# Performance work log

Hardware: AMD Instinct MI355X
Metric: run time of the kernel (lower is better)

Reference implementation:

```python
import jax, jax.numpy as jnp
import numpy as np

EPS_LN = 1e-5
EPS_SM = 1e-16  # PyG softmax denominator epsilon


def setup_inputs() -> dict:
    key = jax.random.key(0)
    k1, k2, k3 = jax.random.split(key, 3)
    N = 100000          # total nodes
    Q, C = 4, 128       # num_querys, hidden_channels
    M = Q * C           # multi_hidden_channels = 512
    B = 512             # batch_size (num graphs)
    x = jax.random.normal(k1, (N, M), dtype=jnp.float32)
    W_nlin = jax.random.normal(k2, (M, M), dtype=jnp.float32) * 0.02
    b_nlin = jnp.zeros((M,), dtype=jnp.float32)
    querys = jnp.ones((Q, C), dtype=jnp.float32)  # q_scale = 1.0 fill
    graph_idx = jnp.sort(jax.random.randint(k3, (N,), 0, B, dtype=jnp.int32))
    return {"x": x, "W_nlin": W_nlin, "b_nlin": b_nlin, "querys": querys,
            "graph_idx": graph_idx, "batch_size": B}


def reference(x, W_nlin, b_nlin, querys, graph_idx, batch_size):
    Q, C = querys.shape
    # nlin: MLP(1 layer, multi_hidden_channels, act=True) -> Linear + ReLU
    h = jax.nn.relu(x @ W_nlin + b_nlin)          # [N, Q*C]
    h = h.reshape(-1, Q, C)                       # [N, Q, C]
    # LayerNorm over hidden_channels, no affine
    mu = jnp.mean(h, axis=-1, keepdims=True)
    var = jnp.mean(jnp.square(h - mu), axis=-1, keepdims=True)
    q = (h - mu) * jax.lax.rsqrt(var + EPS_LN) * querys[None]  # [N, Q, C]
    # segment softmax over nodes within each graph (elementwise in Q, C)
    seg_max = jax.ops.segment_max(q, graph_idx, num_segments=batch_size)  # [B, Q, C]
    e = jnp.exp(q - seg_max[graph_idx])
    seg_sum = jax.ops.segment_sum(e, graph_idx, num_segments=batch_size)
    a = e / (seg_sum[graph_idx] + EPS_SM)         # [N, Q, C]
    # weighted scatter-sum pooling per graph
    r = jax.ops.segment_sum(a * h, graph_idx, num_segments=batch_size)   # [B, Q, C]
    # out_method='lin' with n_agg_trans=0 -> agglin is identity
    return r.reshape(batch_size, -1)              # [B, Q*C]
```

## Files before the change

kernel.cpp:

```cpp
#include <hip/hip_runtime.h>
#include <hip/hip_bf16.h>
#include <stdint.h>

typedef __attribute__((ext_vector_type(8))) short bf16x8;
typedef __attribute__((ext_vector_type(4))) float f32x4;
typedef __attribute__((ext_vector_type(8))) unsigned short ushort8;

__device__ __forceinline__ unsigned short cvt1(float f) {
  union { __hip_bfloat16 b; unsigned short u; } v;
  v.b = __float2bfloat16(f);
  return v.u;
}

__device__ __forceinline__ void gld_lds16(const void* g, void* l) {
  __builtin_amdgcn_global_load_lds(
      (const __attribute__((address_space(1))) unsigned int*)g,
      (__attribute__((address_space(3))) unsigned int*)l,
      16, 0, 0);
}

#define SM_OFS 12.0f

__global__ void cast_wt_kernel(const float* __restrict__ W,
                               unsigned short* __restrict__ wt) {
  int t = blockIdx.x * blockDim.x + threadIdx.x;
  int n = t >> 9;
  int k = t & 511;
  wt[t] = cvt1(W[k * 512 + n]);
}

__global__ __launch_bounds__(256, 4) void gemm_fused_kernel(
    const float* __restrict__ x,
    const unsigned short* __restrict__ wt,
    const float* __restrict__ bias,
    const float* __restrict__ qs,
    const int* __restrict__ gidx,
    float* __restrict__ NU,
    float* __restrict__ SA,
    int N, int mtiles) {
  __shared__ __align__(16) char smem[8192 + 8192];
  char* AsB = smem;
  char* BsB = smem + 8192;

  const int nfull = (mtiles >> 3) << 3;
  const int full_bids = nfull * 4;
  int mtile, ntile;
  {
    const int bid = blockIdx.x;
    if (bid < full_bids) {
      const int chunk = bid >> 5, j = bid & 31;
      mtile = (chunk << 3) + (j & 7);
      ntile = j >> 3;
    } else {
      const int j = bid - full_bids;
      const int rem = mtiles - nfull;
      mtile = nfull + j % rem;
      ntile = j / rem;
    }
  }
  const int m0 = mtile << 6;
  const int n0 = ntile << 7;

  const int tid = threadIdx.x;
  const int lane = tid & 63;
  const int wid = tid >> 6;
  const int wr = wid >> 1;
  const int wc = wid & 1;

  f32x4 acc[2][4];
#pragma unroll
  for (int m = 0; m < 2; m++)
#pragma unroll
    for (int n = 0; n < 4; n++) acc[m][n] = (f32x4){0.f, 0.f, 0.f, 0.f};

  const float* aP[2];
  int aLds[2];
#pragma unroll
  for (int L = 0; L < 2; L++) {
    const int p = (L << 12) + tid * 16;
    const int row = p >> 7;
    const int slot = (p >> 4) & 7;
    const int k4 = slot ^ (row & 7);
    aP[L] = x + (long)min(m0 + row, N - 1) * 512 + k4 * 4;
    aLds[L] = (L << 12) + (wid << 10);
  }

  const unsigned short* bP[2];
  int bLds[2];
#pragma unroll
  for (int L = 0; L < 2; L++) {
    const int p = (L << 12) + tid * 16;
    const int row = p >> 6;
    const int slot = (p >> 4) & 3;
    const int k8 = slot ^ ((row >> 1) & 3);
    bP[L] = wt + (long)(n0 + row) * 512 + k8 * 8;
    bLds[L] = (L << 12) + (wid << 10);
  }

  const int rsel = lane & 15;
  const int k8l = lane >> 4;
  int offA[2], offB[4];
#pragma unroll
  for (int m = 0; m < 2; m++) {
    const int ra = wr * 32 + m * 16 + rsel;
    offA[m] = ra * 128 + (((k8l << 1) ^ (ra & 7)) << 4);
  }
#pragma unroll
  for (int n = 0; n < 4; n++) {
    const int rb = wc * 64 + n * 16 + rsel;
    offB[n] = rb * 64 + ((k8l ^ ((rb >> 1) & 3)) << 4);
  }

#pragma unroll
  for (int t = 0; t < 16; t++) {
#pragma unroll
    for (int L = 0; L < 2; L++) gld_lds16(aP[L] + (t << 5), AsB + aLds[L]);
#pragma unroll
    for (int L = 0; L < 2; L++) gld_lds16(bP[L] + (t << 5), BsB + bLds[L]);
    __syncthreads();

    bf16x8 af[2], bq[4];
#pragma unroll
    for (int m = 0; m < 2; m++) {
      const f32x4 r0 = *(const f32x4*)(AsB + offA[m]);
      const f32x4 r1 = *(const f32x4*)(AsB + (offA[m] ^ 16));
      ushort8 u;
      u[0] = cvt1(r0[0]); u[1] = cvt1(r0[1]);
      u[2] = cvt1(r0[2]); u[3] = cvt1(r0[3]);
      u[4] = cvt1(r1[0]); u[5] = cvt1(r1[1]);
      u[6] = cvt1(r1[2]); u[7] = cvt1(r1[3]);
      af[m] = (bf16x8)u;
    }
#pragma unroll
    for (int n = 0; n < 4; n++) bq[n] = *(const bf16x8*)(BsB + offB[n]);
#pragma unroll
    for (int m = 0; m < 2; m++)
#pragma unroll
      for (int n = 0; n < 4; n++)
        acc[m][n] = __builtin_amdgcn_mfma_f32_16x16x32_bf16(
            af[m], bq[n], acc[m][n], 0, 0, 0);
    __syncthreads();
  }

  int* sgidx = (int*)smem;
  float* sS = (float*)(smem + 256);
  float* sQ = (float*)(smem + 1024);

  if (tid < 64) {
    const long rg = (long)m0 + tid;
    sgidx[tid] = (rg < N) ? gidx[rg] : 0x7fffffff;
  }

  const int colb = n0 + wc * 64 + rsel;
  float bval[4], qsv[4];
#pragma unroll
  for (int n = 0; n < 4; n++) {
    bval[n] = bias[colb + n * 16];
    qsv[n] = qs[colb + n * 16];
  }

#pragma unroll
  for (int m = 0; m < 2; m++) {
#pragma unroll
    for (int i = 0; i < 4; i++) {
      const int row_l = wr * 32 + m * 16 + (k8l << 2) + i;
      float s = 0.f, q = 0.f;
#pragma unroll
      for (int n = 0; n < 4; n++) {
        float v = fmaxf(acc[m][n][i] + bval[n], 0.f);
        s += v;
        q += v * v;
      }
#pragma unroll
      for (int d = 1; d < 16; d <<= 1) {
        s += __shfl_xor(s, d, 64);
        q += __shfl_xor(q, d, 64);
      }
      if (rsel == 0) {
        sS[row_l * 2 + wc] = s;
        sQ[row_l * 2 + wc] = q;
      }
    }
  }
  __syncthreads();

  const int lastv = min(63, (int)((long)N - 1 - (long)m0));
  if (wr * 32 <= lastv) {
    const int gmin = sgidx[wr * 32];
    const int gmax = sgidx[min(wr * 32 + 31, lastv)];
    for (int g = gmin; g <= gmax; ++g) {
      float num[4] = {0.f, 0.f, 0.f, 0.f};
      float den[4] = {0.f, 0.f, 0.f, 0.f};
#pragma unroll
      for (int m = 0; m < 2; m++) {
#pragma unroll
        for (int i = 0; i < 4; i++) {
          const int row_l = wr * 32 + m * 16 + (k8l << 2) + i;
          if (sgidx[row_l] == g) {
            const float s = sS[row_l * 2] + sS[row_l * 2 + 1];
            const float qq = sQ[row_l * 2] + sQ[row_l * 2 + 1];
            const float mean = s * (1.f / 128.f);
            const float var = qq * (1.f / 128.f) - mean * mean;
            const float rstd = rsqrtf(var + 1e-5f);
#pragma unroll
            for (int n = 0; n < 4; n++) {
              const float v = fmaxf(acc[m][n][i] + bval[n], 0.f);
              const float qv = (v - mean) * rstd * qsv[n];
              const float e = __expf(qv - SM_OFS);
              num[n] += e * v;
              den[n] += e;
            }
          }
        }
      }
#pragma unroll
      for (int n = 0; n < 4; n++) {
        num[n] += __shfl_xor(num[n], 16, 64);
        num[n] += __shfl_xor(num[n], 32, 64);
        den[n] += __shfl_xor(den[n], 16, 64);
        den[n] += __shfl_xor(den[n], 32, 64);
      }
      if (k8l == 0) {
#pragma unroll
        for (int n = 0; n < 4; n++) {
          atomicAdd(&NU[(long)g * 512 + colb + n * 16], num[n]);
          atomicAdd(&SA[(long)g * 512 + colb + n * 16], den[n]);
        }
      }
    }
  }
}

__global__ void finalize_kernel(const float* __restrict__ NU,
                                const float* __restrict__ SA,
                                float* __restrict__ out, int total) {
  const int i = blockIdx.x * blockDim.x + threadIdx.x;
  if (i < total) out[i] = NU[i] / (SA[i] + 1e-16f);
}

extern "C" void kernel_launch(void* const* d_in, const int* in_sizes, int n_in,
                              void* d_out, int out_size, void* d_ws, size_t ws_size,
                              hipStream_t stream) {
  const float* x = (const float*)d_in[0];
  const float* W = (const float*)d_in[1];
  const float* bias = (const float*)d_in[2];
  const float* qs = (const float*)d_in[3];
  const int* gidx = (const int*)d_in[4];
  const int N = in_sizes[0] / 512;
  const int B = out_size / 512;
  float* out = (float*)d_out;

  char* ws = (char*)d_ws;
  size_t off = 0;
  auto alloc = [&](size_t bytes) {
    char* p = ws + off;
    off += (bytes + 255) & ~(size_t)255;
    return p;
  };
  unsigned short* wt = (unsigned short*)alloc((size_t)512 * 512 * 2);
  float* accbuf = (float*)alloc((size_t)B * 512 * 2 * sizeof(float));
  float* NU = accbuf;
  float* SA = accbuf + (size_t)B * 512;
  (void)ws_size;

  hipMemsetAsync(accbuf, 0, (size_t)B * 512 * 2 * sizeof(float), stream);
  cast_wt_kernel<<<(512 * 512) / 256, 256, 0, stream>>>(W, wt);
  const int mtiles = (N + 63) / 64;
  gemm_fused_kernel<<<mtiles * 4, 256, 0, stream>>>(x, wt, bias, qs, gidx, NU,
                                                    SA, N, mtiles);
  const int total = B * 512;
  finalize_kernel<<<(total + 255) / 256, 256, 0, stream>>>(NU, SA, out, total);
}
```

Before: 130.2 us.

## Load GEMM operands directly from global into registers, dropping LDS staging

Removes the LDS staging of the x and transposed-weight tiles along with both per-iteration barriers. Each lane now reads its MFMA fragments straight from global memory as float4 and bf16x8 loads. Shared memory shrinks to small epilogue arrays, and the occupancy hint in launch bounds drops from 4 to 3. The trade is that each x row is loaded by both column-half waves and each weight row by both row-half waves, so operand reuse now depends on L1/L2 hits instead of LDS, and global loads are no longer software-pipelined across iterations.

```diff
diff --git a/kernel.cpp b/kernel.cpp
--- a/kernel.cpp
+++ b/kernel.cpp
@@ -10,13 +10,6 @@
   union { __hip_bfloat16 b; unsigned short u; } v;
   v.b = __float2bfloat16(f);
   return v.u;
-}
-
-__device__ __forceinline__ void gld_lds16(const void* g, void* l) {
-  __builtin_amdgcn_global_load_lds(
-      (const __attribute__((address_space(1))) unsigned int*)g,
-      (__attribute__((address_space(3))) unsigned int*)l,
-      16, 0, 0);
 }
 
 #define SM_OFS 12.0f
@@ -29,7 +22,7 @@
   wt[t] = cvt1(W[k * 512 + n]);
 }
 
-__global__ __launch_bounds__(256, 4) void gemm_fused_kernel(
+__global__ __launch_bounds__(256, 3) void gemm_fused_kernel(
     const float* __restrict__ x,
     const unsigned short* __restrict__ wt,
     const float* __restrict__ bias,
@@ -38,9 +31,9 @@
     float* __restrict__ NU,
     float* __restrict__ SA,
     int N, int mtiles) {
-  __shared__ __align__(16) char smem[8192 + 8192];
-  char* AsB = smem;
-  char* BsB = smem + 8192;
+  __shared__ int sgidx[64];
+  __shared__ float sS[128];
+  __shared__ float sQ[128];
 
   const int nfull = (mtiles >> 3) << 3;
   const int full_bids = nfull * 4;
@@ -66,85 +59,56 @@
   const int wid = tid >> 6;
   const int wr = wid >> 1;
   const int wc = wid & 1;
-
-  f32x4 acc[2][4];
-#pragma unroll
-  for (int m = 0; m < 2; m++)
-#pragma unroll
-    for (int n = 0; n < 4; n++) acc[m][n] = (f32x4){0.f, 0.f, 0.f, 0.f};
-
-  const float* aP[2];
-  int aLds[2];
-#pragma unroll
-  for (int L = 0; L < 2; L++) {
-    const int p = (L << 12) + tid * 16;
-    const int row = p >> 7;
-    const int slot = (p >> 4) & 7;
-    const int k4 = slot ^ (row & 7);
-    aP[L] = x + (long)min(m0 + row, N - 1) * 512 + k4 * 4;
-    aLds[L] = (L << 12) + (wid << 10);
-  }
-
-  const unsigned short* bP[2];
-  int bLds[2];
-#pragma unroll
-  for (int L = 0; L < 2; L++) {
-    const int p = (L << 12) + tid * 16;
-    const int row = p >> 6;
-    const int slot = (p >> 4) & 3;
-    const int k8 = slot ^ ((row >> 1) & 3);
-    bP[L] = wt + (long)(n0 + row) * 512 + k8 * 8;
-    bLds[L] = (L << 12) + (wid << 10);
-  }
-
   const int rsel = lane & 15;
   const int k8l = lane >> 4;
-  int offA[2], offB[4];
+
+  const float* aP[2];
 #pragma unroll
   for (int m = 0; m < 2; m++) {
-    const int ra = wr * 32 + m * 16 + rsel;
-    offA[m] = ra * 128 + (((k8l << 1) ^ (ra & 7)) << 4);
-  }
-#pragma unroll
-  for (int n = 0; n < 4; n++) {
-    const int rb = wc * 64 + n * 16 + rsel;
-    offB[n] = rb * 64 + ((k8l ^ ((rb >> 1) & 3)) << 4);
-  }
+    const int row = m0 + wr * 32 + m * 16 + rsel;
+    aP[m] = x + (long)min(row, N - 1) * 512 + (k8l << 3);
+  }
+  const unsigned short* bPt[4];
+#pragma unroll
+  for (int n = 0; n < 4; n++)
+    bPt[n] = wt + (long)(n0 + wc * 64 + n * 16 + rsel) * 512 + (k8l << 3);
+
+  f32x4 acc[2][4];
+#pragma unroll
+  for (int m = 0; m < 2; m++)
+#pragma unroll
+    for (int n = 0; n < 4; n++) acc[m][n] = (f32x4){0.f, 0.f, 0.f, 0.f};
 
 #pragma unroll
   for (int t = 0; t < 16; t++) {
-#pragma unroll
-    for (int L = 0; L < 2; L++) gld_lds16(aP[L] + (t << 5), AsB + aLds[L]);
-#pragma unroll
-    for (int L = 0; L < 2; L++) gld_lds16(bP[L] + (t << 5), BsB + bLds[L]);
-    __syncthreads();
-
-    bf16x8 af[2], bq[4];
+    float4 av[2][2];
+    bf16x8 bv[4];
 #pragma unroll
     for (int m = 0; m < 2; m++) {
-      const f32x4 r0 = *(const f32x4*)(AsB + offA[m]);
-      const f32x4 r1 = *(const f32x4*)(AsB + (offA[m] ^ 16));
+      const float4* ap = (const float4*)(aP[m] + (t << 5));
+      av[m][0] = ap[0];
+      av[m][1] = ap[1];
+    }
+#pragma unroll
+    for (int n = 0; n < 4; n++) bv[n] = *(const bf16x8*)(bPt[n] + (t << 5));
+
+    bf16x8 af[2];
+#pragma unroll
+    for (int m = 0; m < 2; m++) {
       ushort8 u;
-      u[0] = cvt1(r0[0]); u[1] = cvt1(r0[1]);
-      u[2] = cvt1(r0[2]); u[3] = cvt1(r0[3]);
-      u[4] = cvt1(r1[0]); u[5] = cvt1(r1[1]);
-      u[6] = cvt1(r1[2]); u[7] = cvt1(r1[3]);
+      u[0] = cvt1(av[m][0].x); u[1] = cvt1(av[m][0].y);
+      u[2] = cvt1(av[m][0].z); u[3] = cvt1(av[m][0].w);
+      u[4] = cvt1(av[m][1].x); u[5] = cvt1(av[m][1].y);
+      u[6] = cvt1(av[m][1].z); u[7] = cvt1(av[m][1].w);
       af[m] = (bf16x8)u;
     }
-#pragma unroll
-    for (int n = 0; n < 4; n++) bq[n] = *(const bf16x8*)(BsB + offB[n]);
 #pragma unroll
     for (int m = 0; m < 2; m++)
 #pragma unroll
       for (int n = 0; n < 4; n++)
         acc[m][n] = __builtin_amdgcn_mfma_f32_16x16x32_bf16(
-            af[m], bq[n], acc[m][n], 0, 0, 0);
-    __syncthreads();
-  }
-
-  int* sgidx = (int*)smem;
-  float* sS = (float*)(smem + 256);
-  float* sQ = (float*)(smem + 1024);
+            af[m], bv[n], acc[m][n], 0, 0, 0);
+  }
 
   if (tid < 64) {
     const long rg = (long)m0 + tid;
```

Result: slower. 372.5 us (+186.0%).
